# Optimization experiments

Measured on AMD Instinct MI355X. Metric: run time of the kernel, lower is better.

Reference implementation:

```python
import jax, jax.numpy as jnp
import numpy as np


def setup_inputs() -> dict:
    key = jax.random.key(0)
    ks = jax.random.split(key, 3)
    n = 4096
    return {
        "params_batch": jax.random.uniform(ks[0], (n, 15), dtype=jnp.float32),
        "W1": jax.random.normal(ks[1], (8, 32), dtype=jnp.float32) * 0.1,
        "b1": jnp.zeros((32,), dtype=jnp.float32),
        "ln_g": jnp.ones((32,), dtype=jnp.float32),
        "ln_b": jnp.zeros((32,), dtype=jnp.float32),
        "W2": jax.random.normal(ks[2], (32, 16), dtype=jnp.float32) * 0.1,
        "b2": jnp.zeros((16,), dtype=jnp.float32),
    }


def _pairwise_mean(p):
    # p: [n, 15]; returns [n, 8] mean of pairwise features over j != i
    n = p.shape[0]
    t, ra, dec, psi = p[:, 5], p[:, 3], p[:, 4], p[:, 7]
    dt = jnp.abs(t[:, None] - t[None, :])                      # [n, n]
    dra = jnp.abs(ra[:, None] - ra[None, :])
    ddec = jnp.abs(dec[:, None] - dec[None, :])
    sky_sep = jnp.sqrt(dra ** 2 + ddec ** 2)
    m1 = p[:, 0] * 95.0 + 5.0
    m2 = p[:, 1] * 95.0 + 5.0
    mc = (m1 * m2) ** 0.6 / (m1 + m2) ** 0.2                    # chirp mass [n]
    mass_sim = 1.0 / (1.0 + jnp.abs(mc[:, None] - mc[None, :]) / 30.0)
    f_isco = 220.0 / (m1 + m2)
    freq_ov = jnp.exp(-jnp.abs(f_isco[:, None] - f_isco[None, :]) / 100.0)
    dist = p[:, 2] * 2950.0 + 50.0
    dist_ratio = jnp.minimum(dist[:, None], dist[None, :]) / jnp.maximum(dist[:, None], dist[None, :])
    dpsi = jnp.abs(psi[:, None] - psi[None, :])
    feats = jnp.stack([dt, sky_sep, mass_sim, freq_ov, dist_ratio, dpsi, dra, ddec], axis=-1)  # [n, n, 8]
    # diagonal (j == i) contributions: zeros except mass_sim/freq_ov/dist_ratio == 1
    diag = jnp.array([0.0, 0.0, 1.0, 1.0, 1.0, 0.0, 0.0, 0.0], dtype=p.dtype)
    return (feats.sum(axis=1) - diag) / (n - 1)


def reference(params_batch, W1, b1, ln_g, ln_b, W2, b2):
    x = _pairwise_mean(params_batch)          # [n, 8]
    h = x @ W1 + b1                           # [n, 32]
    mu = h.mean(axis=-1, keepdims=True)
    var = h.var(axis=-1, keepdims=True)
    h = (h - mu) * jax.lax.rsqrt(var + 1e-5) * ln_g + ln_b
    h = jax.nn.gelu(h, approximate=False)     # torch GELU default (erf)
    return h @ W2 + b2                        # [n, 16]
```

## Files before the change

### kernel.cpp

```cpp
#include <hip/hip_runtime.h>
#include <math.h>

#define N       4096
#define NPARAM  15
#define NJ      32
#define IB      64
#define JPB     (N / NJ)
#define JPW     (JPB / 4)

__device__ __forceinline__ void derive_params(const float* __restrict__ r, float* o) {
  float m1 = fmaf(r[0], 95.0f, 5.0f);
  float m2 = fmaf(r[1], 95.0f, 5.0f);
  float msum = m1 + m2;
  float mc30 = __builtin_amdgcn_exp2f(
      0.6f * __builtin_amdgcn_logf(m1 * m2)
      - 0.2f * __builtin_amdgcn_logf(msum)
      - 4.906890595608519f);
  o[0] = r[5];
  o[1] = r[3];
  o[2] = r[4];
  o[3] = r[7];
  o[4] = mc30;
  o[5] = 3.1739290899556993f * __builtin_amdgcn_rcpf(msum);
  o[6] = __builtin_amdgcn_logf(fmaf(r[2], 2950.0f, 50.0f));
  o[7] = 0.0f;
}

template <bool PARTIAL>
__global__ __launch_bounds__(256, 8) void pairwise_kernel(
    const float* __restrict__ p, float* __restrict__ out) {
  __shared__ float shj[JPB * 8];
  __shared__ float sacc[4 * IB * 8];
  int t    = threadIdx.x;
  int ib   = blockIdx.x;
  int jb   = blockIdx.y;
  int w    = t >> 6;
  int lane = t & 63;
  int i    = ib * IB + lane;

  if (t < JPB) {
    int j = jb * JPB + t;
    float o[8];
    derive_params(p + (size_t)j * NPARAM, o);
    float4* dst = (float4*)(shj + t * 8);
    dst[0] = make_float4(o[0], o[1], o[2], o[3]);
    dst[1] = make_float4(o[4], o[5], o[6], o[7]);
  }

  float pi[8];
  derive_params(p + (size_t)i * NPARAM, pi);
  float ti = pi[0], rai = pi[1], deci = pi[2], psii = pi[3];
  float mci = pi[4], fi = pi[5], di = pi[6];

  __syncthreads();

  float s0 = 0.f, s1 = 0.f, s2 = 0.f, s3 = 0.f,
        s4 = 0.f, s5 = 0.f, s6 = 0.f, s7 = 0.f;

  const float4* jbase = (const float4*)shj + (size_t)w * JPW * 2;
#pragma unroll 16
  for (int j = 0; j < JPW; j++) {
    float4 a0 = jbase[j * 2];
    float4 a1 = jbase[j * 2 + 1];
    float dra  = rai - a0.y;
    float ddec = deci - a0.z;
    s0 += fabsf(ti - a0.x);
    s5 += fabsf(psii - a0.w);
    s6 += fabsf(dra);
    s7 += fabsf(ddec);
    s1 += __builtin_amdgcn_sqrtf(fmaf(dra, dra, ddec * ddec));
    s2 += __builtin_amdgcn_rcpf(1.0f + fabsf(mci - a1.x));
    s3 += __builtin_amdgcn_exp2f(-fabsf(fi - a1.y));
    s4 += __builtin_amdgcn_exp2f(-fabsf(di - a1.z));
  }

  float4* d = (float4*)(sacc + ((size_t)w * IB + lane) * 8);
  d[0] = make_float4(s0, s1, s2, s3);
  d[1] = make_float4(s4, s5, s6, s7);
  __syncthreads();

#pragma unroll
  for (int k = 0; k < 2; k++) {
    int pidx = t + k * 256;
    float v = sacc[pidx] + sacc[512 + pidx] + sacc[1024 + pidx] + sacc[1536 + pidx];
    if (PARTIAL) {
      out[((size_t)jb * N + (size_t)ib * IB) * 8 + pidx] = v;
    } else {
      atomicAdd(&out[((size_t)ib * IB) * 8 + pidx], v);
    }
  }
}

template <int SLICES>
__global__ __launch_bounds__(256) void mlp_kernel(
    const float* __restrict__ X,
    const float* __restrict__ W1, const float* __restrict__ b1,
    const float* __restrict__ ln_g, const float* __restrict__ ln_b,
    const float* __restrict__ W2, const float* __restrict__ b2,
    float* __restrict__ out) {
  __shared__ float sW1[8 * 32], sW2[32 * 16];
  __shared__ float sb1[32], sg[32], sbb[32], sb2[16];
  __shared__ float sx[16 * 8];
  __shared__ float sh[16 * 32];
  __shared__ float stmp[256];
  int t = threadIdx.x;
  sW1[t] = W1[t];
  sW2[t] = W2[t];
  sW2[t + 256] = W2[t + 256];
  if (t < 32) { sb1[t] = b1[t]; sg[t] = ln_g[t]; sbb[t] = ln_b[t]; }
  if (t < 16) sb2[t] = b2[t];

  int i0 = blockIdx.x * 16;

  {
    int r = t >> 4;
    int q = (t >> 3) & 1;
    int f = t & 7;
    float s = 0.f;
    if (SLICES == 1) {
      if (q == 0) s = X[(size_t)(i0 + r) * 8 + f];
    } else {
      const float* src = X + ((size_t)(q * (SLICES / 2)) * N + (i0 + r)) * 8 + f;
#pragma unroll
      for (int k = 0; k < SLICES / 2; k++) s += src[(size_t)k * N * 8];
    }
    stmp[t] = s;
    __syncthreads();
    if (q == 0) sx[r * 8 + f] = stmp[t] + stmp[t + 8];
  }
  __syncthreads();

  {
    int r = t >> 4;
    int u = t & 15;
    const float diag[8] = {0.f, 0.f, 1.f, 1.f, 1.f, 0.f, 0.f, 0.f};
    const float inv_nm1 = 1.0f / (float)(N - 1);
    float x[8];
#pragma unroll
    for (int k = 0; k < 8; k++) x[k] = (sx[r * 8 + k] - diag[k]) * inv_nm1;

    int o0 = u * 2, o1 = o0 + 1;
    float h0 = sb1[o0], h1 = sb1[o1];
#pragma unroll
    for (int k = 0; k < 8; k++) {
      h0 += x[k] * sW1[k * 32 + o0];
      h1 += x[k] * sW1[k * 32 + o1];
    }

    float sum = h0 + h1;
#pragma unroll
    for (int m = 1; m < 16; m <<= 1) sum += __shfl_xor(sum, m);
    float mu = sum * (1.0f / 32.0f);
    float d0 = h0 - mu, d1 = h1 - mu;
    float vs = d0 * d0 + d1 * d1;
#pragma unroll
    for (int m = 1; m < 16; m <<= 1) vs += __shfl_xor(vs, m);
    float inv = rsqrtf(vs * (1.0f / 32.0f) + 1e-5f);

    float hn0 = d0 * inv * sg[o0] + sbb[o0];
    float hn1 = d1 * inv * sg[o1] + sbb[o1];
    float g0 = 0.5f * hn0 * (1.0f + erff(hn0 * 0.70710678118654752f));
    float g1 = 0.5f * hn1 * (1.0f + erff(hn1 * 0.70710678118654752f));
    sh[r * 32 + o0] = g0;
    sh[r * 32 + o1] = g1;
    __syncthreads();

    float a = sb2[u];
#pragma unroll
    for (int k = 0; k < 32; k++) a += sh[r * 32 + k] * sW2[k * 16 + u];
    out[(size_t)(i0 + r) * 16 + u] = a;
  }
}

extern "C" void kernel_launch(void* const* d_in, const int* in_sizes, int n_in,
                              void* d_out, int out_size, void* d_ws, size_t ws_size,
                              hipStream_t stream) {
  const float* p    = (const float*)d_in[0];
  const float* W1   = (const float*)d_in[1];
  const float* b1   = (const float*)d_in[2];
  const float* ln_g = (const float*)d_in[3];
  const float* ln_b = (const float*)d_in[4];
  const float* W2   = (const float*)d_in[5];
  const float* b2   = (const float*)d_in[6];
  float* out = (float*)d_out;
  float* ws  = (float*)d_ws;

  const size_t need_partial = (size_t)NJ * N * 8 * sizeof(float);
  dim3 grid(N / IB, NJ);
  if (ws_size >= need_partial) {
    pairwise_kernel<true><<<grid, 256, 0, stream>>>(p, ws);
    mlp_kernel<NJ><<<N / 16, 256, 0, stream>>>(ws, W1, b1, ln_g, ln_b, W2, b2, out);
  } else {
    hipMemsetAsync(ws, 0, (size_t)N * 8 * sizeof(float), stream);
    pairwise_kernel<false><<<grid, 256, 0, stream>>>(p, ws);
    mlp_kernel<1><<<N / 16, 256, 0, stream>>>(ws, W1, b1, ln_g, ln_b, W2, b2, out);
  }
}
```

Before: 83.16 us.

## Vectorize pairwise loop with packed f32x2 math and SoA shared layout

Rearranges the per-j derived parameters in shared memory into paired structure-of-arrays buffers so that each load yields the same feature for two j values. The inner loop then uses two-wide float vectors, which lets the compiler emit packed FP32 instructions (v_pk_add/v_pk_mul/v_pk_fma) for the subtract, abs, multiply and accumulate work. The goal is to cut VALU issue count in the compute-bound n^2 loop. Transcendentals remain scalar, the loop is now fully unrolled, and pair-split accumulation changes the summation order slightly.

```diff
diff --git a/kernel.cpp b/kernel.cpp
--- a/kernel.cpp
+++ b/kernel.cpp
@@ -7,6 +7,12 @@
 #define IB      64
 #define JPB     (N / NJ)
 #define JPW     (JPB / 4)
+
+typedef float f32x2 __attribute__((ext_vector_type(2)));
+
+static __device__ __forceinline__ f32x2 abs2(f32x2 v) {
+  return f32x2{fabsf(v.x), fabsf(v.y)};
+}
 
 __device__ __forceinline__ void derive_params(const float* __restrict__ r, float* o) {
   float m1 = fmaf(r[0], 95.0f, 5.0f);
@@ -29,7 +35,10 @@
 template <bool PARTIAL>
 __global__ __launch_bounds__(256, 8) void pairwise_kernel(
     const float* __restrict__ p, float* __restrict__ out) {
-  __shared__ float shj[JPB * 8];
+  __shared__ float4 sAB[JPB / 2];
+  __shared__ float4 sCD[JPB / 2];
+  __shared__ float4 sEF[JPB / 2];
+  __shared__ float2 sG[JPB / 2];
   __shared__ float sacc[4 * IB * 8];
   int t    = threadIdx.x;
   int ib   = blockIdx.x;
@@ -42,9 +51,14 @@
     int j = jb * JPB + t;
     float o[8];
     derive_params(p + (size_t)j * NPARAM, o);
-    float4* dst = (float4*)(shj + t * 8);
-    dst[0] = make_float4(o[0], o[1], o[2], o[3]);
-    dst[1] = make_float4(o[4], o[5], o[6], o[7]);
+    int h = t >> 1, l = t & 1;
+    ((float*)sAB)[h * 4 + l]     = o[0];
+    ((float*)sAB)[h * 4 + 2 + l] = o[1];
+    ((float*)sCD)[h * 4 + l]     = o[2];
+    ((float*)sCD)[h * 4 + 2 + l] = o[3];
+    ((float*)sEF)[h * 4 + l]     = o[4];
+    ((float*)sEF)[h * 4 + 2 + l] = o[5];
+    ((float*)sG)[h * 2 + l]      = o[6];
   }
 
   float pi[8];
@@ -54,25 +68,46 @@
 
   __syncthreads();
 
-  float s0 = 0.f, s1 = 0.f, s2 = 0.f, s3 = 0.f,
-        s4 = 0.f, s5 = 0.f, s6 = 0.f, s7 = 0.f;
-
-  const float4* jbase = (const float4*)shj + (size_t)w * JPW * 2;
-#pragma unroll 16
-  for (int j = 0; j < JPW; j++) {
-    float4 a0 = jbase[j * 2];
-    float4 a1 = jbase[j * 2 + 1];
-    float dra  = rai - a0.y;
-    float ddec = deci - a0.z;
-    s0 += fabsf(ti - a0.x);
-    s5 += fabsf(psii - a0.w);
-    s6 += fabsf(dra);
-    s7 += fabsf(ddec);
-    s1 += __builtin_amdgcn_sqrtf(fmaf(dra, dra, ddec * ddec));
-    s2 += __builtin_amdgcn_rcpf(1.0f + fabsf(mci - a1.x));
-    s3 += __builtin_amdgcn_exp2f(-fabsf(fi - a1.y));
-    s4 += __builtin_amdgcn_exp2f(-fabsf(di - a1.z));
-  }
+  f32x2 a_dt = {0.f, 0.f}, a_sky = {0.f, 0.f}, a_ms = {0.f, 0.f},
+        a_fo = {0.f, 0.f}, a_dr = {0.f, 0.f}, a_ps = {0.f, 0.f},
+        a_ra = {0.f, 0.f}, a_dc = {0.f, 0.f};
+
+  int qbase = w * (JPW / 2);
+#pragma unroll
+  for (int q = 0; q < JPW / 2; q++) {
+    float4 ab = sAB[qbase + q];
+    float4 cd = sCD[qbase + q];
+    float4 ef = sEF[qbase + q];
+    float2 g  = sG[qbase + q];
+    f32x2 tj  = {ab.x, ab.y}, raj = {ab.z, ab.w};
+    f32x2 dcj = {cd.x, cd.y}, psj = {cd.z, cd.w};
+    f32x2 mcj = {ef.x, ef.y}, fj  = {ef.z, ef.w};
+    f32x2 dj  = {g.x, g.y};
+
+    f32x2 dra  = rai - raj;
+    f32x2 ddec = deci - dcj;
+    a_dt += abs2(ti - tj);
+    a_ps += abs2(psii - psj);
+    a_ra += abs2(dra);
+    a_dc += abs2(ddec);
+    f32x2 ss = dra * dra + ddec * ddec;
+    a_sky += f32x2{__builtin_amdgcn_sqrtf(ss.x), __builtin_amdgcn_sqrtf(ss.y)};
+    f32x2 u = 1.0f + abs2(mci - mcj);
+    a_ms += f32x2{__builtin_amdgcn_rcpf(u.x), __builtin_amdgcn_rcpf(u.y)};
+    f32x2 e1 = abs2(fi - fj);
+    a_fo += f32x2{__builtin_amdgcn_exp2f(-e1.x), __builtin_amdgcn_exp2f(-e1.y)};
+    f32x2 e2 = abs2(di - dj);
+    a_dr += f32x2{__builtin_amdgcn_exp2f(-e2.x), __builtin_amdgcn_exp2f(-e2.y)};
+  }
+
+  float s0 = a_dt.x + a_dt.y;
+  float s1 = a_sky.x + a_sky.y;
+  float s2 = a_ms.x + a_ms.y;
+  float s3 = a_fo.x + a_fo.y;
+  float s4 = a_dr.x + a_dr.y;
+  float s5 = a_ps.x + a_ps.y;
+  float s6 = a_ra.x + a_ra.y;
+  float s7 = a_dc.x + a_dc.y;
 
   float4* d = (float4*)(sacc + ((size_t)w * IB + lane) * 8);
   d[0] = make_float4(s0, s1, s2, s3);
```

Result: no change. 82.08 us (-1.3%).
